# Optimization experiments

Measured on AMD Instinct MI355X. Metric: run time of the kernel, lower is better.

The kernel has to match this reference:

```python
import jax, jax.numpy as jnp
import numpy as np

B, T, D, H, O = 256, 512, 256, 512, 1


def setup_inputs() -> dict:
    key = jax.random.key(0)
    ks = jax.random.split(key, 4)
    x = jax.random.normal(ks[0], (B, T, D), dtype=jnp.float32)
    W = jax.random.normal(ks[1], (D, 3 * H), dtype=jnp.float32) * (1.0 / np.sqrt(D))
    U = jax.random.normal(ks[2], (H, 3 * H), dtype=jnp.float32) * (1.0 / np.sqrt(H))
    b = jnp.zeros((3 * H,), dtype=jnp.float32)
    Wd = jax.random.normal(ks[3], (H, O), dtype=jnp.float32) * (1.0 / np.sqrt(H))
    bd = jnp.zeros((O,), dtype=jnp.float32)
    return {"x": x, "W": W, "U": U, "b": b, "Wd": Wd, "bd": bd}


def _gru_last_hidden(x, W, U, b):
    # x: [B, T, D]; returns final hidden state [B, H]
    units = U.shape[0]
    bz, br, bn = b[:units], b[units:2 * units], b[2 * units:]
    Uzr, Un = U[:, :2 * units], U[:, 2 * units:]
    # precompute input projections for all timesteps: [B, T, 3H] -> [T, B, 3H]
    gx = jnp.einsum('btd,dk->tbk', x, W)

    def step(h, gx_t):
        gxz = gx_t[:, :units]
        gxr = gx_t[:, units:2 * units]
        gxn = gx_t[:, 2 * units:]
        gh_zr = h @ Uzr                      # [B, 2H]
        z = jax.nn.sigmoid(gxz + gh_zr[:, :units] + bz)
        r = jax.nn.sigmoid(gxr + gh_zr[:, units:] + br)
        n = jnp.tanh(gxn + (r * h) @ Un + bn)
        h_new = z * h + (1.0 - z) * n
        return h_new, None

    h0 = jnp.zeros((x.shape[0], units), dtype=x.dtype)
    h_last, _ = jax.lax.scan(step, h0, gx)
    return h_last


def reference(x, W, U, b, Wd, bd):
    h_last = _gru_last_hidden(x, W, U, b)  # [B, H]
    return h_last @ Wd + bd                # [B, O]
```

## Files before the change

### kernel.cpp

```cpp
#include <hip/hip_runtime.h>
#include <hip/hip_bf16.h>

typedef __attribute__((ext_vector_type(8))) short short8;
typedef __attribute__((ext_vector_type(4))) float f32x4;
typedef __attribute__((ext_vector_type(4))) unsigned int u32x4;
typedef __attribute__((ext_vector_type(4))) unsigned short u16x4;

#define T_STEPS 512
#define DIM_D 256
#define DIM_H 512
#define NGROUP 8
#define NCOL 32
#define BB 32
#define SLC 16
#define FSTRIDE 32

__device__ __forceinline__ unsigned short f2bf(float f) {
  union { float f; unsigned u; } v; v.f = f;
  unsigned r = v.u + 0x7fffu + ((v.u >> 16) & 1u);
  return (unsigned short)(r >> 16);
}
__device__ __forceinline__ float sigm(float x) { return 1.0f / (1.0f + __expf(-x)); }
__device__ __forceinline__ float tanh_fast(float x) { return 2.0f / (1.0f + __expf(-2.0f * x)) - 1.0f; }

__device__ __forceinline__ void ldg8_bypass(const void* p, u32x4* o) {
  asm volatile(
      "global_load_dwordx4 %0, %8, off sc0 sc1\n\t"
      "global_load_dwordx4 %1, %8, off offset:16 sc0 sc1\n\t"
      "global_load_dwordx4 %2, %8, off offset:32 sc0 sc1\n\t"
      "global_load_dwordx4 %3, %8, off offset:48 sc0 sc1\n\t"
      "global_load_dwordx4 %4, %8, off offset:64 sc0 sc1\n\t"
      "global_load_dwordx4 %5, %8, off offset:80 sc0 sc1\n\t"
      "global_load_dwordx4 %6, %8, off offset:96 sc0 sc1\n\t"
      "global_load_dwordx4 %7, %8, off offset:112 sc0 sc1\n\t"
      "s_waitcnt vmcnt(0)"
      : "=&v"(o[0]), "=&v"(o[1]), "=&v"(o[2]), "=&v"(o[3]),
        "=&v"(o[4]), "=&v"(o[5]), "=&v"(o[6]), "=&v"(o[7])
      : "v"(p)
      : "memory");
}
__device__ __forceinline__ void stg_dx4_bypass(void* p, u32x4 v) {
  asm volatile("global_store_dwordx4 %0, %1, off sc0 sc1" :: "v"(p), "v"(v) : "memory");
}
__device__ __forceinline__ void stg_u32_bypass(void* p, unsigned v) {
  asm volatile("global_store_dword %0, %1, off sc0 sc1" :: "v"(p), "v"(v) : "memory");
}
__device__ __forceinline__ unsigned ldg_u32_bypass(const void* p) {
  unsigned v;
  asm volatile("global_load_dword %0, %1, off sc0 sc1\n\ts_waitcnt vmcnt(0)"
               : "=v"(v) : "v"(p) : "memory");
  return v;
}

__global__ void k_init(unsigned* hx_u32, unsigned* flags) {
  int i = blockIdx.x * 256 + threadIdx.x;
  if (i < 65536) hx_u32[i] = 0u;
  if (i < 2 * 256 * FSTRIDE) flags[i] = 0u;
}

__global__ void k_packW(const float* __restrict__ W, unsigned short* __restrict__ Wt) {
  int n = blockIdx.x, k = threadIdx.x;
  Wt[n * 256 + k] = f2bf(W[(size_t)k * 1536 + n]);
}

__global__ void k_packU(const float* __restrict__ U, unsigned short* __restrict__ Ut) {
  int n = blockIdx.x;
  for (int k = threadIdx.x; k < 512; k += 256)
    Ut[n * 512 + k] = f2bf(U[(size_t)k * 1536 + n]);
}

__global__ void k_out(const float* __restrict__ part, const float* __restrict__ bd,
                      float* __restrict__ out) {
  int b = threadIdx.x;
  float s = bd[0];
  for (int c = 0; c < 32; c++) s += part[c * 256 + b];
  out[b] = s;
}

__global__ void __launch_bounds__(256, 1)
k_gru(const float* __restrict__ x, const float* __restrict__ bias,
      const float* __restrict__ Wd,
      const unsigned short* __restrict__ Wt, const unsigned short* __restrict__ Ut,
      unsigned short* hx, unsigned short* rhx,
      float* part, unsigned* flags) {
  extern __shared__ char smem[];
  char* sUzr = smem;
  char* sUn  = smem + 32768;
  char* sW   = smem + 49152;
  char* sH   = smem + 73728;
  char* sX   = smem + 106496;
  float* sHM = (float*)(smem + 122880);
  char* sG   = smem + 124928;

  const int tid = threadIdx.x;
  const int bid = blockIdx.x;
  const int g = bid & 7;
  const int c = bid >> 3;
  const int w = tid >> 6;
  const int l = tid & 63;
  const int lrow = l & 15;
  const int lk = l >> 4;
  const int n0 = c * SLC;
  const int mt = w & 1;
  const bool zw = (w < 2);

  unsigned* fA = flags + g * 32 * FSTRIDE;
  unsigned* fB = flags + 256 * FSTRIDE + g * 32 * FSTRIDE;

  unsigned short* hx_g  = hx  + (size_t)g * (BB * DIM_H);
  unsigned short* rhx_g = rhx + (size_t)g * (BB * DIM_H);

  for (int q = tid; q < 2048; q += 256) {
    int n = q >> 6, ch = q & 63;
    int grow = (n < 16) ? (n0 + n) : (DIM_H + n0 + (n - 16));
    u32x4 v = *(const u32x4*)(Ut + (size_t)grow * DIM_H + ch * 8);
    *(u32x4*)(sUzr + n * 1024 + ((ch * 16) ^ ((n & 7) << 4))) = v;
  }
  for (int q = tid; q < 1024; q += 256) {
    int n = q >> 6, ch = q & 63;
    int grow = 2 * DIM_H + n0 + n;
    u32x4 v = *(const u32x4*)(Ut + (size_t)grow * DIM_H + ch * 8);
    *(u32x4*)(sUn + n * 1024 + ((ch * 16) ^ ((n & 7) << 4))) = v;
  }
  for (int q = tid; q < 1536; q += 256) {
    int n = q >> 5, ch = q & 31;
    int grow = (n < 16) ? (n0 + n) : (n < 32 ? (DIM_H + n0 + (n - 16))
                                             : (2 * DIM_H + n0 + (n - 32)));
    u32x4 v = *(const u32x4*)(Wt + (size_t)grow * DIM_D + ch * 8);
    *(u32x4*)(sW + n * 512 + ((ch * 16) ^ ((n & 7) << 4))) = v;
  }
  sHM[tid] = 0.0f; sHM[tid + 256] = 0.0f;
  const float bz_l = bias[n0 + lrow];
  const float br_l = bias[DIM_H + n0 + lrow];
  const float bn_l = bias[2 * DIM_H + n0 + lrow];
  __syncthreads();

  f32x4 azr, an;

  auto stage_x = [&](int t) {
    const int xr = tid >> 3;
    const int xj = (tid & 7) * 32;
    const float* xp = x + ((size_t)(g * BB + xr) * T_STEPS + t) * DIM_D + xj;
#pragma unroll
    for (int i = 0; i < 8; i++) {
      float4 v = ((const float4*)xp)[i];
      u16x4 h4 = { f2bf(v.x), f2bf(v.y), f2bf(v.z), f2bf(v.w) };
      int kb = (xj + i * 4) * 2;
      *(u16x4*)(sX + xr * 512 + (kb ^ ((xr & 7) << 4))) = h4;
    }
  };

  auto w_mfma = [&]() {
    float bini = zw ? bz_l : br_l;
    f32x4 t0 = { bini, bini, bini, bini };
    azr = t0;
    f32x4 t1 = { bn_l, bn_l, bn_l, bn_l };
    an = t1;
    const int arow = mt * 16 + lrow;
    const int nzr = zw ? lrow : (16 + lrow);
    const int nnn = 32 + lrow;
#pragma unroll
    for (int ks = 0; ks < 8; ks++) {
      int kb = ks * 64 + lk * 16;
      short8 a = *(const short8*)(sX + arow * 512 + (kb ^ ((arow & 7) << 4)));
      short8 b0 = *(const short8*)(sW + nzr * 512 + (kb ^ ((nzr & 7) << 4)));
      azr = __builtin_amdgcn_mfma_f32_16x16x32_bf16(a, b0, azr, 0, 0, 0);
      if (zw) {
        short8 b1 = *(const short8*)(sW + nnn * 512 + (kb ^ ((nnn & 7) << 4)));
        an = __builtin_amdgcn_mfma_f32_16x16x32_bf16(a, b1, an, 0, 0, 0);
      }
    }
  };

  auto stage_gl = [&](const unsigned short* src_base) {
    const int hr = tid >> 3;
    const int hc = (tid & 7) * 128;
    const char* s0 = (const char*)(src_base + hr * DIM_H) + hc;
    u32x4 v[8];
    ldg8_bypass(s0, v);
    char* dst = sH + hr * 1024;
    const int sw = (hr & 7) << 4;
#pragma unroll
    for (int i = 0; i < 8; i++)
      *(u32x4*)(dst + ((hc + i * 16) ^ sw)) = v[i];
  };

  auto uzr_mfma = [&]() {
    const int arow = mt * 16 + lrow;
    const int n = zw ? lrow : (16 + lrow);
#pragma unroll
    for (int ks = 0; ks < 16; ks++) {
      int kb = ks * 64 + lk * 16;
      short8 a = *(const short8*)(sH + arow * 1024 + (kb ^ ((arow & 7) << 4)));
      short8 b8 = *(const short8*)(sUzr + n * 1024 + (kb ^ ((n & 7) << 4)));
      azr = __builtin_amdgcn_mfma_f32_16x16x32_bf16(a, b8, azr, 0, 0, 0);
    }
  };

  auto un_mfma = [&]() {
    const int arow = mt * 16 + lrow;
#pragma unroll
    for (int ks = 0; ks < 16; ks++) {
      int kb = ks * 64 + lk * 16;
      short8 a = *(const short8*)(sH + arow * 1024 + (kb ^ ((arow & 7) << 4)));
      short8 b8 = *(const short8*)(sUn + lrow * 1024 + (kb ^ ((lrow & 7) << 4)));
      an = __builtin_amdgcn_mfma_f32_16x16x32_bf16(a, b8, an, 0, 0, 0);
    }
  };

  auto publish = [&](unsigned short* dst_g, unsigned* f, unsigned e, bool do_poll) {
    const int row = l >> 1, hf = l & 1;
    u32x4 v = *(const u32x4*)(sG + row * 32 + hf * 16);
    stg_dx4_bypass((char*)dst_g + row * 1024 + n0 * 2 + hf * 16, v);
    asm volatile("s_waitcnt vmcnt(0)" ::: "memory");
    if (l == 0) stg_u32_bypass(f + c * FSTRIDE, e);
    if (do_poll && l < 32) {
      while (ldg_u32_bypass(f + l * FSTRIDE) < e) __builtin_amdgcn_s_sleep(1);
    }
  };

  stage_x(0);
  __syncthreads();
  w_mfma();

  for (int t = 0; t < T_STEPS; t++) {
    const unsigned e = (unsigned)(t + 1);
    stage_gl(hx_g);
    __syncthreads();
    uzr_mfma();
    if (!zw) {
#pragma unroll
      for (int j = 0; j < 4; j++) {
        int row = mt * 16 + lk * 4 + j;
        float rv = sigm(azr[j]);
        ((unsigned short*)sG)[row * 16 + lrow] = f2bf(rv * sHM[row * 16 + lrow]);
      }
    }
    __syncthreads();
    if (w == 0) publish(rhx_g, fA, e, true);
    __syncthreads();

    stage_gl(rhx_g);
    __syncthreads();
    if (zw) {
      un_mfma();
#pragma unroll
      for (int j = 0; j < 4; j++) {
        int row = mt * 16 + lk * 4 + j;
        float zv = sigm(azr[j]);
        float nv = tanh_fast(an[j]);
        float hv = sHM[row * 16 + lrow];
        float hn = zv * hv + (1.0f - zv) * nv;
        sHM[row * 16 + lrow] = hn;
        ((unsigned short*)sG)[row * 16 + lrow] = f2bf(hn);
      }
    }
    __syncthreads();
    if (t + 1 == T_STEPS) break;
    if (w == 0) publish(hx_g, fB, e, false);
    stage_x(t + 1);
    __syncthreads();
    w_mfma();
    if (w == 0 && l < 32) {
      while (ldg_u32_bypass(fB + l * FSTRIDE) < e) __builtin_amdgcn_s_sleep(1);
    }
    __syncthreads();
  }

  if (tid < BB) {
    float s = 0.0f;
#pragma unroll
    for (int i = 0; i < SLC; i++) s += sHM[tid * 16 + i] * Wd[n0 + i];
    part[c * 256 + g * BB + tid] = s;
  }
}

extern "C" void kernel_launch(void* const* d_in, const int* in_sizes, int n_in,
                              void* d_out, int out_size, void* d_ws, size_t ws_size,
                              hipStream_t stream) {
  const float* x    = (const float*)d_in[0];
  const float* W    = (const float*)d_in[1];
  const float* U    = (const float*)d_in[2];
  const float* bias = (const float*)d_in[3];
  const float* Wd   = (const float*)d_in[4];
  const float* bd   = (const float*)d_in[5];
  float* out = (float*)d_out;
  char* ws = (char*)d_ws;

  unsigned short* Wt  = (unsigned short*)(ws + 0);
  unsigned short* Ut  = (unsigned short*)(ws + 786432);
  unsigned short* hx  = (unsigned short*)(ws + 2359296);
  unsigned short* rhx = (unsigned short*)(ws + 2621440);
  float* part         = (float*)(ws + 2883584);
  unsigned* flags     = (unsigned*)(ws + 2916352);

  hipFuncSetAttribute((const void*)k_gru, hipFuncAttributeMaxDynamicSharedMemorySize, 125952);

  k_init<<<256, 256, 0, stream>>>((unsigned*)hx, flags);
  k_packW<<<1536, 256, 0, stream>>>(W, Wt);
  k_packU<<<1536, 256, 0, stream>>>(U, Ut);
  k_gru<<<256, 256, 125952, stream>>>(x, bias, Wd, Wt, Ut, hx, rhx, part, flags);
  k_out<<<1, 256, 0, stream>>>(part, bd, out);
}
```

Baseline: 5.359 ms.

## Publish GRU gate outputs directly from compute waves with per-wave flags

Compute waves now write their bf16 r*h and new-h values straight to global memory and each sets its own flag, so flags grow to 64 per group. This removes the LDS staging buffer, two block barriers per step and the serialized publish by wave 0. Polling is split across waves (wave 0 for fA, wave 2 for fB) so it can overlap other work. The cost is uncoalesced 2-byte global stores instead of 16-byte vector stores, and twice as many flags to poll.

```diff
diff --git a/kernel.cpp b/kernel.cpp
--- a/kernel.cpp
+++ b/kernel.cpp
@@ -39,8 +39,8 @@
       : "v"(p)
       : "memory");
 }
-__device__ __forceinline__ void stg_dx4_bypass(void* p, u32x4 v) {
-  asm volatile("global_store_dwordx4 %0, %1, off sc0 sc1" :: "v"(p), "v"(v) : "memory");
+__device__ __forceinline__ void stg_u16_bypass(void* p, unsigned v) {
+  asm volatile("global_store_short %0, %1, off sc0 sc1" :: "v"(p), "v"(v) : "memory");
 }
 __device__ __forceinline__ void stg_u32_bypass(void* p, unsigned v) {
   asm volatile("global_store_dword %0, %1, off sc0 sc1" :: "v"(p), "v"(v) : "memory");
@@ -55,7 +55,7 @@
 __global__ void k_init(unsigned* hx_u32, unsigned* flags) {
   int i = blockIdx.x * 256 + threadIdx.x;
   if (i < 65536) hx_u32[i] = 0u;
-  if (i < 2 * 256 * FSTRIDE) flags[i] = 0u;
+  if (i < 2 * NGROUP * 64 * FSTRIDE) flags[i] = 0u;
 }
 
 __global__ void k_packW(const float* __restrict__ W, unsigned short* __restrict__ Wt) {
@@ -90,7 +90,6 @@
   char* sH   = smem + 73728;
   char* sX   = smem + 106496;
   float* sHM = (float*)(smem + 122880);
-  char* sG   = smem + 124928;
 
   const int tid = threadIdx.x;
   const int bid = blockIdx.x;
@@ -104,8 +103,8 @@
   const int mt = w & 1;
   const bool zw = (w < 2);
 
-  unsigned* fA = flags + g * 32 * FSTRIDE;
-  unsigned* fB = flags + 256 * FSTRIDE + g * 32 * FSTRIDE;
+  unsigned* fA = flags + g * 64 * FSTRIDE;
+  unsigned* fB = flags + NGROUP * 64 * FSTRIDE + g * 64 * FSTRIDE;
 
   unsigned short* hx_g  = hx  + (size_t)g * (BB * DIM_H);
   unsigned short* rhx_g = rhx + (size_t)g * (BB * DIM_H);
@@ -208,23 +207,13 @@
     }
   };
 
-  auto publish = [&](unsigned short* dst_g, unsigned* f, unsigned e, bool do_poll) {
-    const int row = l >> 1, hf = l & 1;
-    u32x4 v = *(const u32x4*)(sG + row * 32 + hf * 16);
-    stg_dx4_bypass((char*)dst_g + row * 1024 + n0 * 2 + hf * 16, v);
-    asm volatile("s_waitcnt vmcnt(0)" ::: "memory");
-    if (l == 0) stg_u32_bypass(f + c * FSTRIDE, e);
-    if (do_poll && l < 32) {
-      while (ldg_u32_bypass(f + l * FSTRIDE) < e) __builtin_amdgcn_s_sleep(1);
-    }
-  };
-
   stage_x(0);
   __syncthreads();
   w_mfma();
 
   for (int t = 0; t < T_STEPS; t++) {
     const unsigned e = (unsigned)(t + 1);
+
     stage_gl(hx_g);
     __syncthreads();
     uzr_mfma();
@@ -233,11 +222,14 @@
       for (int j = 0; j < 4; j++) {
         int row = mt * 16 + lk * 4 + j;
         float rv = sigm(azr[j]);
-        ((unsigned short*)sG)[row * 16 + lrow] = f2bf(rv * sHM[row * 16 + lrow]);
-      }
-    }
-    __syncthreads();
-    if (w == 0) publish(rhx_g, fA, e, true);
+        stg_u16_bypass(rhx_g + row * DIM_H + n0 + lrow,
+                       (unsigned)f2bf(rv * sHM[row * 16 + lrow]));
+      }
+      asm volatile("s_waitcnt vmcnt(0)" ::: "memory");
+      if (l == 0) stg_u32_bypass(fA + ((c << 1) | (w & 1)) * FSTRIDE, e);
+    } else if (w == 0) {
+      while (ldg_u32_bypass(fA + l * FSTRIDE) < e) __builtin_amdgcn_s_sleep(1);
+    }
     __syncthreads();
 
     stage_gl(rhx_g);
@@ -252,16 +244,19 @@
         float hv = sHM[row * 16 + lrow];
         float hn = zv * hv + (1.0f - zv) * nv;
         sHM[row * 16 + lrow] = hn;
-        ((unsigned short*)sG)[row * 16 + lrow] = f2bf(hn);
-      }
-    }
-    __syncthreads();
-    if (t + 1 == T_STEPS) break;
-    if (w == 0) publish(hx_g, fB, e, false);
+        if (t + 1 < T_STEPS)
+          stg_u16_bypass(hx_g + row * DIM_H + n0 + lrow, (unsigned)f2bf(hn));
+      }
+      if (t + 1 < T_STEPS) {
+        asm volatile("s_waitcnt vmcnt(0)" ::: "memory");
+        if (l == 0) stg_u32_bypass(fB + ((c << 1) | w) * FSTRIDE, e);
+      }
+    }
+    if (t + 1 == T_STEPS) { __syncthreads(); break; }
     stage_x(t + 1);
     __syncthreads();
     w_mfma();
-    if (w == 0 && l < 32) {
+    if (w == 2) {
       while (ldg_u32_bypass(fB + l * FSTRIDE) < e) __builtin_amdgcn_s_sleep(1);
     }
     __syncthreads();
@@ -294,11 +289,11 @@
   float* part         = (float*)(ws + 2883584);
   unsigned* flags     = (unsigned*)(ws + 2916352);
 
-  hipFuncSetAttribute((const void*)k_gru, hipFuncAttributeMaxDynamicSharedMemorySize, 125952);
+  hipFuncSetAttribute((const void*)k_gru, hipFuncAttributeMaxDynamicSharedMemorySize, 124928);
 
   k_init<<<256, 256, 0, stream>>>((unsigned*)hx, flags);
   k_packW<<<1536, 256, 0, stream>>>(W, Wt);
   k_packU<<<1536, 256, 0, stream>>>(U, Ut);
-  k_gru<<<256, 256, 125952, stream>>>(x, bias, Wd, Wt, Ut, hx, rhx, part, flags);
+  k_gru<<<256, 256, 124928, stream>>>(x, bias, Wd, Wt, Ut, hx, rhx, part, flags);
   k_out<<<1, 256, 0, stream>>>(part, bd, out);
 }
```

Measured after the change: 5.234 ms. 2.3% less time.
